# Performance work log

Hardware: AMD Instinct MI355X
Metric: run time of the kernel (lower is better)

## Reference

```python
import jax, jax.numpy as jnp
import numpy as np

N = 50000      # nodes
E = 800000     # edges (avg degree 16)
DIN = 128
DOUT = 128
L = 8          # num GCN2Conv layers
ALPHA = 0.1
THETA = 0.5


def setup_inputs() -> dict:
    key = jax.random.key(0)
    ks = jax.random.split(key, 5)
    x = jax.random.normal(ks[0], (N, DIN), jnp.float32)
    edge_index = jax.random.randint(ks[1], (2, E), 0, N, dtype=jnp.int64)
    # pre-normalized adjacency weights (normalize=False in GCN2Conv -> adj_t already normalized)
    edge_weight = jax.random.uniform(ks[2], (E,), jnp.float32) / 16.0
    W_lin = jax.random.normal(ks[3], (DIN, DOUT), jnp.float32) / np.sqrt(DIN).astype(np.float32)
    b_lin = jnp.zeros((DOUT,), jnp.float32)
    W_convs = jax.random.normal(ks[4], (L, DOUT, DOUT), jnp.float32) / np.sqrt(DOUT).astype(np.float32)
    return {"x": x, "edge_weight": edge_weight, "W_lin": W_lin, "b_lin": b_lin,
            "W_convs": W_convs, "edge_index": edge_index}


def reference(x, edge_weight, W_lin, b_lin, W_convs, edge_index):
    src, dst = edge_index[0], edge_index[1]
    # betas for GCN2Conv layer l (1-indexed): beta_l = log(theta/l + 1)
    betas = np.log(THETA / np.arange(1, L + 1) + 1.0).astype(np.float32)
    # x = lins(x).relu(); dropout p=0 is a no-op
    x0 = jax.nn.relu(x @ W_lin + b_lin)          # [N, DOUT]
    h = x0
    for l in range(L):
        # sparse propagate: agg = A @ h  (SpMM via gather + segment_sum)
        agg = jax.ops.segment_sum(h[src] * edge_weight[:, None], dst, num_segments=N)
        # initial-residual mixing
        m = (1.0 - ALPHA) * agg + ALPHA * x0
        # identity mapping (shared_weights): out = (1-beta)*m + beta*(m @ W)
        h = jax.nn.relu((1.0 - betas[l]) * m + betas[l] * (m @ W_convs[l]))
    return h
```

## Files before the change

### kernel.cpp

```cpp
#include <hip/hip_runtime.h>
#include <math.h>

#define N_NODES 50000
#define N_EDGES 800000
#define DIM 128
#define PAD 128

typedef __attribute__((ext_vector_type(8))) short short8;
typedef __attribute__((ext_vector_type(4))) float floatx4;

__device__ __forceinline__ unsigned short f32_to_bf16(float f) {
    unsigned int u = __float_as_uint(f);
    u += 0x7fffu + ((u >> 16) & 1u);
    return (unsigned short)(u >> 16);
}
__device__ __forceinline__ float bf16_to_f32(unsigned short h) {
    return __uint_as_float((unsigned int)h << 16);
}


__global__ __launch_bounds__(256) void scatter_pad(const int* __restrict__ src,
                                                   const int* __restrict__ dst,
                                                   const float* __restrict__ ew,
                                                   int* __restrict__ cnt,
                                                   int2* __restrict__ bucket) {
    int e = blockIdx.x * 256 + threadIdx.x;
    if (e < N_EDGES) {
        int d = dst[e];
        int pos = atomicAdd(&cnt[d], 1);
        if (pos < PAD) {
            int2 p; p.x = src[e]; p.y = __float_as_int(ew[e]);
            bucket[(size_t)d * PAD + pos] = p;
        }
    }
}


__global__ __launch_bounds__(256) void spmm8(const unsigned short* __restrict__ hB,
                                             const unsigned short* __restrict__ x0B,
                                             const int* __restrict__ cnt,
                                             const int2* __restrict__ bucket,
                                             unsigned short* __restrict__ mB) {
    int node = blockIdx.x * 4 + (threadIdx.x >> 6);
    int lane = threadIdx.x & 63;
    int eg = lane >> 4;
    int fb = (lane & 15) * 8;
    int end = min(cnt[node], PAD);
    const int2* ep = bucket + (size_t)node * PAD;
    float acc[8] = {0.f, 0.f, 0.f, 0.f, 0.f, 0.f, 0.f, 0.f};
    if (end > 0) {
        int last = end - 1;
        for (int i = 0; i < end; i += 16) {
            int i0 = i + eg, i1 = i0 + 4, i2 = i0 + 8, i3 = i0 + 12;
            int2 e0 = ep[min(i0, last)];
            int2 e1 = ep[min(i1, last)];
            int2 e2 = ep[min(i2, last)];
            int2 e3 = ep[min(i3, last)];
            short8 r0 = *(const short8*)(const void*)(hB + (size_t)e0.x * DIM + fb);
            short8 r1 = *(const short8*)(const void*)(hB + (size_t)e1.x * DIM + fb);
            short8 r2 = *(const short8*)(const void*)(hB + (size_t)e2.x * DIM + fb);
            short8 r3 = *(const short8*)(const void*)(hB + (size_t)e3.x * DIM + fb);
            float w0 = (i0 < end) ? __int_as_float(e0.y) : 0.f;
            float w1 = (i1 < end) ? __int_as_float(e1.y) : 0.f;
            float w2 = (i2 < end) ? __int_as_float(e2.y) : 0.f;
            float w3 = (i3 < end) ? __int_as_float(e3.y) : 0.f;
#pragma unroll
            for (int j = 0; j < 8; j++) {
                acc[j] = fmaf(w0, bf16_to_f32((unsigned short)r0[j]), acc[j]);
                acc[j] = fmaf(w1, bf16_to_f32((unsigned short)r1[j]), acc[j]);
                acc[j] = fmaf(w2, bf16_to_f32((unsigned short)r2[j]), acc[j]);
                acc[j] = fmaf(w3, bf16_to_f32((unsigned short)r3[j]), acc[j]);
            }
        }
    }
#pragma unroll
    for (int j = 0; j < 8; j++) {
        acc[j] += __shfl_down(acc[j], 32);
        acc[j] += __shfl_down(acc[j], 16);
    }
    if (lane < 16) {
        size_t off = (size_t)node * DIM + fb;
        short8 xv = *(const short8*)(const void*)(x0B + off);
        short8 o;
#pragma unroll
        for (int j = 0; j < 8; j++)
            o[j] = (short)f32_to_bf16(0.9f * acc[j]
                                      + 0.1f * bf16_to_f32((unsigned short)xv[j]));
        *(short8*)(void*)(mB + off) = o;
    }
}


template <bool AF32>
__global__ __launch_bounds__(256) void gemm128(const void* __restrict__ Av,
                                               const float* __restrict__ W,
                                               const float* __restrict__ bias,
                                               float* __restrict__ outF,
                                               unsigned short* __restrict__ outB,
                                               float cm, float cg) {
    __shared__ unsigned short WT[128][136];
    for (int idx = threadIdx.x; idx < 128 * 128; idx += 256) {
        int k = idx >> 7, n = idx & 127;
        float wv = cg * W[idx] + ((n == k) ? cm : 0.f);
        WT[n][k] = f32_to_bf16(wv);
    }
    __syncthreads();

    int wave = threadIdx.x >> 6;
    int lane = threadIdx.x & 63;
    int r0 = (blockIdx.x * 4 + wave) * 16;
    if (r0 >= N_NODES) return;

    int mrow = lane & 15;
    int quad = lane >> 4;

    floatx4 acc[8];
#pragma unroll
    for (int t = 0; t < 8; t++) acc[t] = {0.f, 0.f, 0.f, 0.f};

#pragma unroll
    for (int k0 = 0; k0 < 128; k0 += 32) {
        short8 a;
        if constexpr (AF32) {
            const float* arow = (const float*)Av + (size_t)(r0 + mrow) * DIM;
            floatx4 alo = *(const floatx4*)(const void*)(arow + k0 + quad * 8);
            floatx4 ahi = *(const floatx4*)(const void*)(arow + k0 + quad * 8 + 4);
#pragma unroll
            for (int j = 0; j < 4; j++) a[j] = (short)f32_to_bf16(alo[j]);
#pragma unroll
            for (int j = 0; j < 4; j++) a[4 + j] = (short)f32_to_bf16(ahi[j]);
        } else {
            const unsigned short* arow = (const unsigned short*)Av + (size_t)(r0 + mrow) * DIM;
            a = *(const short8*)(const void*)(arow + k0 + quad * 8);
        }
#pragma unroll
        for (int t = 0; t < 8; t++) {
            short8 b = *(const short8*)(const void*)(&WT[t * 16 + mrow][k0 + quad * 8]);
            acc[t] = __builtin_amdgcn_mfma_f32_16x16x32_bf16(a, b, acc[t], 0, 0, 0);
        }
    }

#pragma unroll
    for (int t = 0; t < 8; t++) {
        int col = t * 16 + mrow;
        float bv = bias ? bias[col] : 0.f;
#pragma unroll
        for (int i = 0; i < 4; i++) {
            int row = r0 + quad * 4 + i;
            size_t off = (size_t)row * DIM + col;
            float v = fmaxf(acc[t][i] + bv, 0.f);
            if (outF) outF[off] = v;
            if (outB) outB[off] = f32_to_bf16(v);
        }
    }
}


extern "C" void kernel_launch(void* const* d_in, const int* in_sizes, int n_in,
                              void* d_out, int out_size, void* d_ws, size_t ws_size,
                              hipStream_t stream) {
    const float* x    = (const float*)d_in[0];
    const float* ew   = (const float*)d_in[1];
    const float* Wlin = (const float*)d_in[2];
    const float* blin = (const float*)d_in[3];
    const float* Wcv  = (const float*)d_in[4];
    const int* eidx = (const int*)d_in[5];
    const int* esrc = eidx;
    const int* edst = eidx + N_EDGES;
    float* out = (float*)d_out;

    char* ws = (char*)d_ws;
    unsigned short* x0B = (unsigned short*)(ws);
    unsigned short* mB  = (unsigned short*)(ws + 12800000);
    unsigned short* hB  = (unsigned short*)(ws + 25600000);
    int* cnt            = (int*)(ws + 38400000);
    int2* bucket        = (int2*)(ws + 38600064);

    const int grid = (N_NODES + 63) / 64;

    gemm128<true><<<grid, 256, 0, stream>>>(x, Wlin, blin, nullptr, x0B, 0.f, 1.f);

    (void)hipMemsetAsync(cnt, 0, N_NODES * sizeof(int), stream);
    scatter_pad<<<(N_EDGES + 255) / 256, 256, 0, stream>>>(esrc, edst, ew, cnt, bucket);

    const unsigned short* hin = x0B;
    for (int l = 0; l < 8; l++) {
        spmm8<<<N_NODES / 4, 256, 0, stream>>>(hin, x0B, cnt, bucket, mB);
        float beta = logf(0.5f / (float)(l + 1) + 1.f);
        gemm128<false><<<grid, 256, 0, stream>>>(mB, Wcv + (size_t)l * DIM * DIM, nullptr,
                                                 (l == 7) ? out : nullptr,
                                                 (l < 7) ? hB : nullptr,
                                                 1.f - beta, beta);
        hin = hB;
    }
}
```

Before: 500.6 us.

## Fuse edge bucketing with input GEMM and partition atomics by destination range

Merges the edge-scatter kernel and the initial linear GEMM into one launch. Blocks are split by index: the first set scatters edges, the rest run the input projection. Each edge chunk is now processed by 8 blocks, and each block handles only destinations in its own node range, so concurrent atomics land on nearby counters and writes hit a smaller region. In exchange, every edge's dst is read 8 times, and the scatter blocks also reserve the GEMM's shared-memory tile, which may lower occupancy for the scatter portion.

```diff
diff --git a/kernel.cpp b/kernel.cpp
--- a/kernel.cpp
+++ b/kernel.cpp
@@ -5,6 +5,11 @@
 #define N_EDGES 800000
 #define DIM 128
 #define PAD 128
+#define NPART 8
+#define PART_SZ 6250
+#define SCAT_CHUNKS 3125
+#define SCAT_BLOCKS (SCAT_CHUNKS * NPART)
+#define GEMM_BLOCKS 782
 
 typedef __attribute__((ext_vector_type(8))) short short8;
 typedef __attribute__((ext_vector_type(4))) float floatx4;
@@ -19,19 +24,98 @@
 }
 
 
-__global__ __launch_bounds__(256) void scatter_pad(const int* __restrict__ src,
-                                                   const int* __restrict__ dst,
-                                                   const float* __restrict__ ew,
-                                                   int* __restrict__ cnt,
-                                                   int2* __restrict__ bucket) {
-    int e = blockIdx.x * 256 + threadIdx.x;
-    if (e < N_EDGES) {
-        int d = dst[e];
-        int pos = atomicAdd(&cnt[d], 1);
-        if (pos < PAD) {
-            int2 p; p.x = src[e]; p.y = __float_as_int(ew[e]);
-            bucket[(size_t)d * PAD + pos] = p;
-        }
+template <bool AF32>
+__device__ __forceinline__ void gemm_body(int bid, const void* __restrict__ Av,
+                                          const float* __restrict__ W,
+                                          const float* __restrict__ bias,
+                                          float* __restrict__ outF,
+                                          unsigned short* __restrict__ outB,
+                                          float cm, float cg,
+                                          unsigned short (*WT)[136]) {
+    for (int idx = threadIdx.x; idx < 128 * 128; idx += 256) {
+        int k = idx >> 7, n = idx & 127;
+        float wv = cg * W[idx] + ((n == k) ? cm : 0.f);
+        WT[n][k] = f32_to_bf16(wv);
+    }
+    __syncthreads();
+
+    int wave = threadIdx.x >> 6;
+    int lane = threadIdx.x & 63;
+    int r0 = (bid * 4 + wave) * 16;
+    if (r0 >= N_NODES) return;
+
+    int mrow = lane & 15;
+    int quad = lane >> 4;
+
+    floatx4 acc[8];
+#pragma unroll
+    for (int t = 0; t < 8; t++) acc[t] = {0.f, 0.f, 0.f, 0.f};
+
+#pragma unroll
+    for (int k0 = 0; k0 < 128; k0 += 32) {
+        short8 a;
+        if constexpr (AF32) {
+            const float* arow = (const float*)Av + (size_t)(r0 + mrow) * DIM;
+            floatx4 alo = *(const floatx4*)(const void*)(arow + k0 + quad * 8);
+            floatx4 ahi = *(const floatx4*)(const void*)(arow + k0 + quad * 8 + 4);
+#pragma unroll
+            for (int j = 0; j < 4; j++) a[j] = (short)f32_to_bf16(alo[j]);
+#pragma unroll
+            for (int j = 0; j < 4; j++) a[4 + j] = (short)f32_to_bf16(ahi[j]);
+        } else {
+            const unsigned short* arow = (const unsigned short*)Av + (size_t)(r0 + mrow) * DIM;
+            a = *(const short8*)(const void*)(arow + k0 + quad * 8);
+        }
+#pragma unroll
+        for (int t = 0; t < 8; t++) {
+            short8 b = *(const short8*)(const void*)(&WT[t * 16 + mrow][k0 + quad * 8]);
+            acc[t] = __builtin_amdgcn_mfma_f32_16x16x32_bf16(a, b, acc[t], 0, 0, 0);
+        }
+    }
+
+#pragma unroll
+    for (int t = 0; t < 8; t++) {
+        int col = t * 16 + mrow;
+        float bv = bias ? bias[col] : 0.f;
+#pragma unroll
+        for (int i = 0; i < 4; i++) {
+            int row = r0 + quad * 4 + i;
+            size_t off = (size_t)row * DIM + col;
+            float v = fmaxf(acc[t][i] + bv, 0.f);
+            if (outF) outF[off] = v;
+            if (outB) outB[off] = f32_to_bf16(v);
+        }
+    }
+}
+
+
+__global__ __launch_bounds__(256) void scatter_gemm0(const int* __restrict__ src,
+                                                     const int* __restrict__ dst,
+                                                     const float* __restrict__ ew,
+                                                     int* __restrict__ cnt,
+                                                     int2* __restrict__ bucket,
+                                                     const float* __restrict__ x,
+                                                     const float* __restrict__ Wlin,
+                                                     const float* __restrict__ blin,
+                                                     unsigned short* __restrict__ x0B) {
+    __shared__ unsigned short WT[128][136];
+    if (blockIdx.x < SCAT_BLOCKS) {
+        int part = blockIdx.x & (NPART - 1);
+        int e = (blockIdx.x >> 3) * 256 + threadIdx.x;
+        int lo = part * PART_SZ;
+        if (e < N_EDGES) {
+            int d = dst[e];
+            if ((unsigned)(d - lo) < PART_SZ) {
+                int pos = atomicAdd(&cnt[d], 1);
+                if (pos < PAD) {
+                    int2 p; p.x = src[e]; p.y = __float_as_int(ew[e]);
+                    bucket[(size_t)d * PAD + pos] = p;
+                }
+            }
+        }
+    } else {
+        gemm_body<true>(blockIdx.x - SCAT_BLOCKS, x, Wlin, blin,
+                        nullptr, x0B, 0.f, 1.f, WT);
     }
 }
 
@@ -91,68 +175,13 @@
 }
 
 
-template <bool AF32>
-__global__ __launch_bounds__(256) void gemm128(const void* __restrict__ Av,
-                                               const float* __restrict__ W,
-                                               const float* __restrict__ bias,
-                                               float* __restrict__ outF,
-                                               unsigned short* __restrict__ outB,
-                                               float cm, float cg) {
+__global__ __launch_bounds__(256) void gemm_layer(const unsigned short* __restrict__ A,
+                                                  const float* __restrict__ W,
+                                                  float* __restrict__ outF,
+                                                  unsigned short* __restrict__ outB,
+                                                  float cm, float cg) {
     __shared__ unsigned short WT[128][136];
-    for (int idx = threadIdx.x; idx < 128 * 128; idx += 256) {
-        int k = idx >> 7, n = idx & 127;
-        float wv = cg * W[idx] + ((n == k) ? cm : 0.f);
-        WT[n][k] = f32_to_bf16(wv);
-    }
-    __syncthreads();
-
-    int wave = threadIdx.x >> 6;
-    int lane = threadIdx.x & 63;
-    int r0 = (blockIdx.x * 4 + wave) * 16;
-    if (r0 >= N_NODES) return;
-
-    int mrow = lane & 15;
-    int quad = lane >> 4;
-
-    floatx4 acc[8];
-#pragma unroll
-    for (int t = 0; t < 8; t++) acc[t] = {0.f, 0.f, 0.f, 0.f};
-
-#pragma unroll
-    for (int k0 = 0; k0 < 128; k0 += 32) {
-        short8 a;
-        if constexpr (AF32) {
-            const float* arow = (const float*)Av + (size_t)(r0 + mrow) * DIM;
-            floatx4 alo = *(const floatx4*)(const void*)(arow + k0 + quad * 8);
-            floatx4 ahi = *(const floatx4*)(const void*)(arow + k0 + quad * 8 + 4);
-#pragma unroll
-            for (int j = 0; j < 4; j++) a[j] = (short)f32_to_bf16(alo[j]);
-#pragma unroll
-            for (int j = 0; j < 4; j++) a[4 + j] = (short)f32_to_bf16(ahi[j]);
-        } else {
-            const unsigned short* arow = (const unsigned short*)Av + (size_t)(r0 + mrow) * DIM;
-            a = *(const short8*)(const void*)(arow + k0 + quad * 8);
-        }
-#pragma unroll
-        for (int t = 0; t < 8; t++) {
-            short8 b = *(const short8*)(const void*)(&WT[t * 16 + mrow][k0 + quad * 8]);
-            acc[t] = __builtin_amdgcn_mfma_f32_16x16x32_bf16(a, b, acc[t], 0, 0, 0);
-        }
-    }
-
-#pragma unroll
-    for (int t = 0; t < 8; t++) {
-        int col = t * 16 + mrow;
-        float bv = bias ? bias[col] : 0.f;
-#pragma unroll
-        for (int i = 0; i < 4; i++) {
-            int row = r0 + quad * 4 + i;
-            size_t off = (size_t)row * DIM + col;
-            float v = fmaxf(acc[t][i] + bv, 0.f);
-            if (outF) outF[off] = v;
-            if (outB) outB[off] = f32_to_bf16(v);
-        }
-    }
+    gemm_body<false>(blockIdx.x, A, W, nullptr, outF, outB, cm, cg, WT);
 }
 
 
@@ -176,21 +205,18 @@
     int* cnt            = (int*)(ws + 38400000);
     int2* bucket        = (int2*)(ws + 38600064);
 
-    const int grid = (N_NODES + 63) / 64;
-
-    gemm128<true><<<grid, 256, 0, stream>>>(x, Wlin, blin, nullptr, x0B, 0.f, 1.f);
-
     (void)hipMemsetAsync(cnt, 0, N_NODES * sizeof(int), stream);
-    scatter_pad<<<(N_EDGES + 255) / 256, 256, 0, stream>>>(esrc, edst, ew, cnt, bucket);
+    scatter_gemm0<<<SCAT_BLOCKS + GEMM_BLOCKS, 256, 0, stream>>>(
+        esrc, edst, ew, cnt, bucket, x, Wlin, blin, x0B);
 
     const unsigned short* hin = x0B;
     for (int l = 0; l < 8; l++) {
         spmm8<<<N_NODES / 4, 256, 0, stream>>>(hin, x0B, cnt, bucket, mB);
         float beta = logf(0.5f / (float)(l + 1) + 1.f);
-        gemm128<false><<<grid, 256, 0, stream>>>(mB, Wcv + (size_t)l * DIM * DIM, nullptr,
-                                                 (l == 7) ? out : nullptr,
-                                                 (l < 7) ? hB : nullptr,
-                                                 1.f - beta, beta);
+        gemm_layer<<<GEMM_BLOCKS, 256, 0, stream>>>(mB, Wcv + (size_t)l * DIM * DIM,
+                                                    (l == 7) ? out : nullptr,
+                                                    (l < 7) ? hB : nullptr,
+                                                    1.f - beta, beta);
         hin = hB;
     }
 }
```

Measured after the change: 503.1 us. Within noise of the previous version (+0.5%).
